# Performance work log

Hardware: AMD Instinct MI355X
Metric: run time of the kernel (lower is better)

Reference implementation:

```python
import jax, jax.numpy as jnp
import numpy as np

IN_FEATURES = 4096
OUT_FEATURES = 4096
BLOCK_SIZE = 16
E2M1_VALUES = jnp.array([0.0, 0.5, 1.0, 1.5, 2.0, 3.0, 4.0, 6.0], dtype=jnp.float32)


def dequantize_nvfp4(weight_packed, weight_scales, out_features, in_features, block_size, dtype):
    # Unpack two 4-bit codes per byte: even positions = high nibble, odd = low nibble
    p = weight_packed.astype(jnp.int32)
    high = (p >> 4) & 15
    low = p & 15
    unpacked = jnp.stack([high, low], axis=-1).reshape(-1)  # [out*in]
    sign = ((unpacked >> 3) & 1).astype(dtype)
    mag_code = unpacked & 7
    magnitude = E2M1_VALUES.astype(dtype)[mag_code]
    vals = jnp.where(sign == 1, -magnitude, magnitude)
    # Expand per-block E4M3 scales (repeat_interleave)
    scales_expanded = jnp.repeat(weight_scales.astype(dtype), block_size)
    w = vals * scales_expanded
    return w.reshape(out_features, in_features)


def setup_inputs() -> dict:
    key = jax.random.key(0)
    k1, k2, k3, k4 = jax.random.split(key, 4)
    x = jax.random.normal(k1, (4, 2048, IN_FEATURES), dtype=jnp.float32)
    weight_packed = jax.random.randint(k2, (OUT_FEATURES * IN_FEATURES // 2,), 0, 256, dtype=jnp.int32)
    weight_scales = jax.random.uniform(k3, (OUT_FEATURES * IN_FEATURES // BLOCK_SIZE,), dtype=jnp.float32)
    bias = jax.random.normal(k4, (OUT_FEATURES,), dtype=jnp.float32)
    return {"x": x, "weight_packed": weight_packed, "weight_scales": weight_scales, "bias": bias}


def reference(x, weight_packed, weight_scales, bias):
    w = dequantize_nvfp4(weight_packed, weight_scales, OUT_FEATURES, IN_FEATURES, BLOCK_SIZE, x.dtype)
    # F.linear: y = x @ w.T + bias
    return jnp.einsum('bsi,oi->bso', x, w) + bias
```

## Files before the change

### kernel.cpp

```cpp
#include <hip/hip_runtime.h>
#include <cstdint>
#include <cstddef>

#define MDIM 8192
#define NDIM 4096
#define KDIM 4096

typedef __attribute__((ext_vector_type(8))) __bf16 bf16x8;
typedef __attribute__((ext_vector_type(4))) float floatx4;

typedef __attribute__((address_space(3))) void lds_t;
typedef __attribute__((address_space(1))) void glb_t;

__device__ __forceinline__ unsigned short f32_to_bf16(float f) {
  unsigned int u = __float_as_uint(f);
  u += 0x7FFFu + ((u >> 16) & 1u);
  return (unsigned short)(u >> 16);
}

__device__ __forceinline__ float fp4_mag(int c) {
  int e = (c >> 1) & 3, m = c & 1;
  int sh = e ? (e - 1) : 0;
  return e ? 0.5f * (float)((2 + m) << sh) : 0.5f * (float)m;
}

__global__ __launch_bounds__(256) void conv_x_kernel(const float* __restrict__ x,
                                                     unsigned short* __restrict__ xb) {
  const int t = blockIdx.x * 256 + threadIdx.x;
  const float4* src = (const float4*)x + (size_t)t * 2;
  float4 a = src[0], b = src[1];
  union { unsigned short us[8]; uint4 u4; } o;
  o.us[0] = f32_to_bf16(a.x); o.us[1] = f32_to_bf16(a.y);
  o.us[2] = f32_to_bf16(a.z); o.us[3] = f32_to_bf16(a.w);
  o.us[4] = f32_to_bf16(b.x); o.us[5] = f32_to_bf16(b.y);
  o.us[6] = f32_to_bf16(b.z); o.us[7] = f32_to_bf16(b.w);
  ((uint4*)xb)[t] = o.u4;
}

__global__ __launch_bounds__(256) void dequant_kernel(const int* __restrict__ packed,
                                                      const float* __restrict__ scales,
                                                      unsigned short* __restrict__ wb) {
  const int t = blockIdx.x * 256 + threadIdx.x;
  const int4* p = (const int4*)packed + (size_t)t * 2;
  int4 pa = p[0], pb = p[1];
  float s = scales[t];
  int bytes[8] = {pa.x, pa.y, pa.z, pa.w, pb.x, pb.y, pb.z, pb.w};
  union { unsigned short us[16]; uint4 u4[2]; } o;
#pragma unroll
  for (int i = 0; i < 8; ++i) {
    int by = bytes[i] & 255;
    int hi = by >> 4, lo = by & 15;
    float vh = fp4_mag(hi & 7) * s; if (hi & 8) vh = -vh;
    float vl = fp4_mag(lo & 7) * s; if (lo & 8) vl = -vl;
    o.us[2 * i]     = f32_to_bf16(vh);
    o.us[2 * i + 1] = f32_to_bf16(vl);
  }
  uint4* dst = (uint4*)(wb + (size_t)t * 16);
  dst[0] = o.u4[0]; dst[1] = o.u4[1];
}

__global__ __launch_bounds__(512, 2) void gemm256_kernel(const __bf16* __restrict__ A,
                                                         const __bf16* __restrict__ B,
                                                         const float* __restrict__ bias,
                                                         float* __restrict__ C) {
  __shared__ __bf16 ldsbuf[65536];
  __bf16* As = ldsbuf;
  __bf16* Bs = ldsbuf + 32768;

  const int t = threadIdx.x;
  const int wave = t >> 6, lane = t & 63;
  const int quad = lane >> 4, r16 = lane & 15;
  const int wr = wave >> 2, wc = wave & 3;

  const int bid = blockIdx.x;
  const int wg = (bid & 7) * 64 + (bid >> 3);
  const int m0 = (wg >> 4) * 256, n0 = (wg & 15) * 256;

  const int swzS = ((t >> 3) & 7) << 4;
  const int b0 = (t * 16) ^ swzS;
  const int b1 = (8192 + t * 16) ^ swzS;
  const int row0 = b0 >> 6, col0 = (b0 & 63) >> 1;
  const int row1 = b1 >> 6, col1 = (b1 & 63) >> 1;

  const __bf16* pa0 = A + (size_t)(m0 + row0) * KDIM + col0;
  const __bf16* pa1 = A + (size_t)(m0 + row1) * KDIM + col1;
  const __bf16* pb0 = B + (size_t)(n0 + row0) * KDIM + col0;
  const __bf16* pb1 = B + (size_t)(n0 + row1) * KDIM + col1;

  const int swzR = ((r16 >> 1) & 7) << 4;
  const int offAe = ((((wr * 128 + r16) * 64) + quad * 16) ^ swzR) >> 1;
  const int offBe = ((((wc * 64  + r16) * 64) + quad * 16) ^ swzR) >> 1;

  floatx4 acc[8][4] = {};

#pragma unroll
  for (int p = 0; p < 3; ++p) {
    __bf16* _ab = As + p * 8192;
    __bf16* _bb = Bs + p * 8192;
    __builtin_amdgcn_global_load_lds((const glb_t*)(pa0 + p * 32), (lds_t*)(_ab + wave * 512), 16, 0, 0);
    __builtin_amdgcn_global_load_lds((const glb_t*)(pa1 + p * 32), (lds_t*)(_ab + 4096 + wave * 512), 16, 0, 0);
    __builtin_amdgcn_global_load_lds((const glb_t*)(pb0 + p * 32), (lds_t*)(_bb + wave * 512), 16, 0, 0);
    __builtin_amdgcn_global_load_lds((const glb_t*)(pb1 + p * 32), (lds_t*)(_bb + 4096 + wave * 512), 16, 0, 0);
  }
  asm volatile("s_waitcnt vmcnt(8)" ::: "memory");
  __builtin_amdgcn_s_barrier();

  const __bf16* sa0 = pa0 + 96;
  const __bf16* sa1 = pa1 + 96;
  const __bf16* sb0 = pb0 + 96;
  const __bf16* sb1 = pb1 + 96;

#define TILE(TT, DO_STAGE, VMASM) do {                                            \
    const __bf16* _a = As + ((TT) & 3) * 8192;                                    \
    const __bf16* _b = Bs + ((TT) & 3) * 8192;                                    \
    __bf16* _sa = As + (((TT) + 3) & 3) * 8192;                                   \
    __bf16* _sb = Bs + (((TT) + 3) & 3) * 8192;                                   \
    bf16x8 af[4], bfv[4];                                                         \
                                               \
    _Pragma("unroll")                                                             \
    for (int i = 0; i < 4; ++i) af[i] = *(const bf16x8*)(_a + offAe + i * 512);   \
    _Pragma("unroll")                                                             \
    for (int j = 0; j < 4; ++j) bfv[j] = *(const bf16x8*)(_b + offBe + j * 512);  \
    if (DO_STAGE) {                                                               \
      __builtin_amdgcn_global_load_lds((const glb_t*)sa0, (lds_t*)(_sa + wave * 512), 16, 0, 0);        \
      __builtin_amdgcn_global_load_lds((const glb_t*)sa1, (lds_t*)(_sa + 4096 + wave * 512), 16, 0, 0); \
    }                                                                             \
    __builtin_amdgcn_s_barrier();                                                 \
    asm volatile("s_waitcnt lgkmcnt(0)" ::: "memory");                            \
    __builtin_amdgcn_sched_barrier(0);                                            \
    __builtin_amdgcn_s_setprio(1);                                                \
    _Pragma("unroll")                                                             \
    for (int i = 0; i < 4; ++i) {                                                 \
      _Pragma("unroll")                                                           \
      for (int j = 0; j < 4; ++j)                                                 \
        acc[i][j] = __builtin_amdgcn_mfma_f32_16x16x32_bf16(af[i], bfv[j], acc[i][j], 0, 0, 0); \
    }                                                                             \
    __builtin_amdgcn_s_setprio(0);                                                \
    __builtin_amdgcn_s_barrier();                                                 \
                                               \
    _Pragma("unroll")                                                             \
    for (int i = 0; i < 4; ++i) af[i] = *(const bf16x8*)(_a + offAe + (4 + i) * 512); \
    if (DO_STAGE) {                                                               \
      __builtin_amdgcn_global_load_lds((const glb_t*)sb0, (lds_t*)(_sb + wave * 512), 16, 0, 0);        \
      __builtin_amdgcn_global_load_lds((const glb_t*)sb1, (lds_t*)(_sb + 4096 + wave * 512), 16, 0, 0); \
    }                                                                             \
    __builtin_amdgcn_s_barrier();                                                 \
    asm volatile("s_waitcnt lgkmcnt(0)" ::: "memory");                            \
    __builtin_amdgcn_sched_barrier(0);                                            \
    __builtin_amdgcn_s_setprio(1);                                                \
    _Pragma("unroll")                                                             \
    for (int i = 0; i < 4; ++i) {                                                 \
      _Pragma("unroll")                                                           \
      for (int j = 0; j < 4; ++j)                                                 \
        acc[4 + i][j] = __builtin_amdgcn_mfma_f32_16x16x32_bf16(af[i], bfv[j], acc[4 + i][j], 0, 0, 0); \
    }                                                                             \
    __builtin_amdgcn_s_setprio(0);                                                \
    VMASM;                                                                        \
    __builtin_amdgcn_s_barrier();                                                 \
  } while (0)

  for (int T = 0; T < 125; ++T) {
    TILE(T, true, asm volatile("s_waitcnt vmcnt(8)" ::: "memory"));
    sa0 += 32; sa1 += 32; sb0 += 32; sb1 += 32;
  }
  TILE(125, false, asm volatile("s_waitcnt vmcnt(4)" ::: "memory"));
  TILE(126, false, asm volatile("s_waitcnt vmcnt(0)" ::: "memory"));
  TILE(127, false, (void)0);

#undef TILE

  float bv[4];
#pragma unroll
  for (int j = 0; j < 4; ++j) bv[j] = bias[n0 + wc * 64 + j * 16 + r16];
#pragma unroll
  for (int i = 0; i < 8; ++i) {
    const int gm = m0 + wr * 128 + i * 16 + quad * 4;
#pragma unroll
    for (int j = 0; j < 4; ++j) {
      float* cp = C + (size_t)gm * NDIM + (n0 + wc * 64 + j * 16 + r16);
#pragma unroll
      for (int r = 0; r < 4; ++r)
        cp[(size_t)r * NDIM] = acc[i][j][r] + bv[j];
    }
  }
}

__global__ __launch_bounds__(256) void fused_fallback(const float* __restrict__ x,
                                                      const int* __restrict__ packed,
                                                      const float* __restrict__ scales,
                                                      const float* __restrict__ bias,
                                                      float* __restrict__ out) {
  const int n = blockIdx.x * 256 + threadIdx.x;
  const int m = blockIdx.y;
  const float* xr = x + (size_t)m * KDIM;
  const int* pr = packed + (size_t)n * (KDIM / 2);
  const float* sc = scales + (size_t)n * (KDIM / 16);
  float acc = 0.f;
  for (int kb = 0; kb < KDIM / 16; ++kb) {
    float s = sc[kb];
    float part = 0.f;
#pragma unroll
    for (int i = 0; i < 8; ++i) {
      int by = pr[kb * 8 + i] & 255;
      int hi = by >> 4, lo = by & 15;
      float vh = fp4_mag(hi & 7); if (hi & 8) vh = -vh;
      float vl = fp4_mag(lo & 7); if (lo & 8) vl = -vl;
      part += xr[kb * 16 + 2 * i] * vh + xr[kb * 16 + 2 * i + 1] * vl;
    }
    acc += s * part;
  }
  out[(size_t)m * NDIM + n] = acc + bias[n];
}

extern "C" void kernel_launch(void* const* d_in, const int* in_sizes, int n_in,
                              void* d_out, int out_size, void* d_ws, size_t ws_size,
                              hipStream_t stream) {
  const float* x      = (const float*)d_in[0];
  const int*   packed = (const int*)d_in[1];
  const float* scales = (const float*)d_in[2];
  const float* bias   = (const float*)d_in[3];
  float* out = (float*)d_out;

  const size_t needA = (size_t)MDIM * KDIM * 2;
  const size_t needW = (size_t)NDIM * KDIM * 2;

  if (ws_size >= needA + needW) {
    unsigned short* xb = (unsigned short*)d_ws;
    unsigned short* wb = (unsigned short*)((char*)d_ws + needA);
    conv_x_kernel<<<(MDIM * KDIM / 8) / 256, 256, 0, stream>>>(x, xb);
    dequant_kernel<<<(NDIM * KDIM / 16) / 256, 256, 0, stream>>>(packed, scales, wb);
    dim3 grid((MDIM / 256) * (NDIM / 256));
    gemm256_kernel<<<grid, 512, 0, stream>>>((const __bf16*)xb, (const __bf16*)wb, bias, out);
  } else {
    dim3 grid(NDIM / 256, MDIM);
    fused_fallback<<<grid, 256, 0, stream>>>(x, packed, scales, bias, out);
  }
}
```

Measured before the change: 493.2 us.

## Software-pipeline LDS fragment reads into the previous MFMA phase

```diff
diff --git a/kernel.cpp b/kernel.cpp
--- a/kernel.cpp
+++ b/kernel.cpp
@@ -5,6 +5,7 @@
 #define MDIM 8192
 #define NDIM 4096
 #define KDIM 4096
+
 
 typedef __attribute__((ext_vector_type(8))) __bf16 bf16x8;
 typedef __attribute__((ext_vector_type(4))) float floatx4;
@@ -92,6 +93,7 @@
   const int offBe = ((((wc * 64  + r16) * 64) + quad * 16) ^ swzR) >> 1;
 
   floatx4 acc[8][4] = {};
+  bf16x8 afA[4], afB[4], bfv0[4], bfv1[4];
 
 #pragma unroll
   for (int p = 0; p < 3; ++p) {
@@ -105,69 +107,93 @@
   asm volatile("s_waitcnt vmcnt(8)" ::: "memory");
   __builtin_amdgcn_s_barrier();
 
+#pragma unroll
+  for (int i = 0; i < 4; ++i) afA[i] = *(const bf16x8*)(As + offAe + i * 512);
+#pragma unroll
+  for (int j = 0; j < 4; ++j) bfv0[j] = *(const bf16x8*)(Bs + offBe + j * 512);
+
   const __bf16* sa0 = pa0 + 96;
   const __bf16* sa1 = pa1 + 96;
   const __bf16* sb0 = pb0 + 96;
   const __bf16* sb1 = pb1 + 96;
 
-#define TILE(TT, DO_STAGE, VMASM) do {                                            \
+#define VM6 asm volatile("s_waitcnt vmcnt(6)" ::: "memory")
+#define VM4 asm volatile("s_waitcnt vmcnt(4)" ::: "memory")
+#define VM0 asm volatile("s_waitcnt vmcnt(0)" ::: "memory")
+#define VMNONE (void)0
+
+#define PH_A(TT, BV, DO_STAGE, SOFF, VMASM) do {                                  \
     const __bf16* _a = As + ((TT) & 3) * 8192;                                    \
-    const __bf16* _b = Bs + ((TT) & 3) * 8192;                                    \
     __bf16* _sa = As + (((TT) + 3) & 3) * 8192;                                   \
-    __bf16* _sb = Bs + (((TT) + 3) & 3) * 8192;                                   \
-    bf16x8 af[4], bfv[4];                                                         \
-                                               \
     _Pragma("unroll")                                                             \
-    for (int i = 0; i < 4; ++i) af[i] = *(const bf16x8*)(_a + offAe + i * 512);   \
-    _Pragma("unroll")                                                             \
-    for (int j = 0; j < 4; ++j) bfv[j] = *(const bf16x8*)(_b + offBe + j * 512);  \
+    for (int i = 0; i < 4; ++i) afB[i] = *(const bf16x8*)(_a + offAe + (4 + i) * 512); \
     if (DO_STAGE) {                                                               \
-      __builtin_amdgcn_global_load_lds((const glb_t*)sa0, (lds_t*)(_sa + wave * 512), 16, 0, 0);        \
-      __builtin_amdgcn_global_load_lds((const glb_t*)sa1, (lds_t*)(_sa + 4096 + wave * 512), 16, 0, 0); \
-    }                                                                             \
-    __builtin_amdgcn_s_barrier();                                                 \
-    asm volatile("s_waitcnt lgkmcnt(0)" ::: "memory");                            \
+      __builtin_amdgcn_global_load_lds((const glb_t*)(sa0 + (SOFF)), (lds_t*)(_sa + wave * 512), 16, 0, 0);        \
+      __builtin_amdgcn_global_load_lds((const glb_t*)(sa1 + (SOFF)), (lds_t*)(_sa + 4096 + wave * 512), 16, 0, 0); \
+    }                                                                             \
     __builtin_amdgcn_sched_barrier(0);                                            \
     __builtin_amdgcn_s_setprio(1);                                                \
     _Pragma("unroll")                                                             \
     for (int i = 0; i < 4; ++i) {                                                 \
       _Pragma("unroll")                                                           \
       for (int j = 0; j < 4; ++j)                                                 \
-        acc[i][j] = __builtin_amdgcn_mfma_f32_16x16x32_bf16(af[i], bfv[j], acc[i][j], 0, 0, 0); \
+        acc[i][j] = __builtin_amdgcn_mfma_f32_16x16x32_bf16(afA[i], BV[j], acc[i][j], 0, 0, 0); \
     }                                                                             \
     __builtin_amdgcn_s_setprio(0);                                                \
+    __builtin_amdgcn_sched_barrier(0);                                            \
+    VMASM;                                                                        \
     __builtin_amdgcn_s_barrier();                                                 \
-                                               \
-    _Pragma("unroll")                                                             \
-    for (int i = 0; i < 4; ++i) af[i] = *(const bf16x8*)(_a + offAe + (4 + i) * 512); \
+  } while (0)
+
+#define PH_B(TT, BV, BVN, DO_STAGE, DO_NEXT, DO_BAR, SOFF) do {                   \
+    const __bf16* _na = As + (((TT) + 1) & 3) * 8192;                             \
+    const __bf16* _nb = Bs + (((TT) + 1) & 3) * 8192;                             \
+    __bf16* _sb = Bs + (((TT) + 3) & 3) * 8192;                                   \
+    if (DO_NEXT) {                                                                \
+      _Pragma("unroll")                                                           \
+      for (int i = 0; i < 4; ++i) afA[i] = *(const bf16x8*)(_na + offAe + i * 512);  \
+      _Pragma("unroll")                                                           \
+      for (int j = 0; j < 4; ++j) BVN[j] = *(const bf16x8*)(_nb + offBe + j * 512);  \
+    }                                                                             \
     if (DO_STAGE) {                                                               \
-      __builtin_amdgcn_global_load_lds((const glb_t*)sb0, (lds_t*)(_sb + wave * 512), 16, 0, 0);        \
-      __builtin_amdgcn_global_load_lds((const glb_t*)sb1, (lds_t*)(_sb + 4096 + wave * 512), 16, 0, 0); \
-    }                                                                             \
-    __builtin_amdgcn_s_barrier();                                                 \
-    asm volatile("s_waitcnt lgkmcnt(0)" ::: "memory");                            \
+      __builtin_amdgcn_global_load_lds((const glb_t*)(sb0 + (SOFF)), (lds_t*)(_sb + wave * 512), 16, 0, 0);        \
+      __builtin_amdgcn_global_load_lds((const glb_t*)(sb1 + (SOFF)), (lds_t*)(_sb + 4096 + wave * 512), 16, 0, 0); \
+    }                                                                             \
     __builtin_amdgcn_sched_barrier(0);                                            \
     __builtin_amdgcn_s_setprio(1);                                                \
     _Pragma("unroll")                                                             \
     for (int i = 0; i < 4; ++i) {                                                 \
       _Pragma("unroll")                                                           \
       for (int j = 0; j < 4; ++j)                                                 \
-        acc[4 + i][j] = __builtin_amdgcn_mfma_f32_16x16x32_bf16(af[i], bfv[j], acc[4 + i][j], 0, 0, 0); \
+        acc[4 + i][j] = __builtin_amdgcn_mfma_f32_16x16x32_bf16(afB[i], BV[j], acc[4 + i][j], 0, 0, 0); \
     }                                                                             \
     __builtin_amdgcn_s_setprio(0);                                                \
-    VMASM;                                                                        \
-    __builtin_amdgcn_s_barrier();                                                 \
+    __builtin_amdgcn_sched_barrier(0);                                            \
+    if (DO_BAR) __builtin_amdgcn_s_barrier();                                     \
   } while (0)
 
-  for (int T = 0; T < 125; ++T) {
-    TILE(T, true, asm volatile("s_waitcnt vmcnt(8)" ::: "memory"));
-    sa0 += 32; sa1 += 32; sb0 += 32; sb1 += 32;
-  }
-  TILE(125, false, asm volatile("s_waitcnt vmcnt(4)" ::: "memory"));
-  TILE(126, false, asm volatile("s_waitcnt vmcnt(0)" ::: "memory"));
-  TILE(127, false, (void)0);
-
-#undef TILE
+  for (int T = 0; T < 124; T += 2) {
+    PH_A(T,     bfv0, true, 0,  VM6);
+    PH_B(T,     bfv0, bfv1, true, true, true, 0);
+    PH_A(T + 1, bfv1, true, 32, VM6);
+    PH_B(T + 1, bfv1, bfv0, true, true, true, 32);
+    sa0 += 64; sa1 += 64; sb0 += 64; sb1 += 64;
+  }
+  PH_A(124, bfv0, true,  0, VM6);
+  PH_B(124, bfv0, bfv1, true,  true, true, 0);
+  PH_A(125, bfv1, false, 0, VM4);
+  PH_B(125, bfv1, bfv0, false, true, true, 0);
+  PH_A(126, bfv0, false, 0, VM0);
+  PH_B(126, bfv0, bfv1, false, true, true, 0);
+  PH_A(127, bfv1, false, 0, VMNONE);
+  PH_B(127, bfv1, bfv0, false, false, false, 0);
+
+#undef PH_A
+#undef PH_B
+#undef VM6
+#undef VM4
+#undef VM0
+#undef VMNONE
 
   float bv[4];
 #pragma unroll
```

New measurement: 479.2 us. -2.8%, faster.
